# Performance work log

Hardware: AMD Instinct MI355X
Metric: run time of the kernel (lower is better)

Reference implementation:

```python
import jax, jax.numpy as jnp
import numpy as np

B, C, H, W = 8, 16, 64, 64
O = 32
K = 3
STRIDE = 1
HO = (H - K) // STRIDE + 1  # 62
WO = (W - K) // STRIDE + 1  # 62
BIAS_VAL = 0.1


def setup_inputs() -> dict:
    key = jax.random.key(0)
    k1, k2 = jax.random.split(key)
    x = jax.random.normal(k1, (B, C, H, W), dtype=jnp.float32)
    # per-location weights: (1, O, C, Ho, Wo, K*K) in torch; drop leading 1
    weight = jax.random.normal(k2, (O, C, HO, WO, K * K), dtype=jnp.float32)
    bias = jnp.full((1, O, HO, WO), BIAS_VAL, dtype=jnp.float32)
    return {"x": x, "weight": weight, "bias": bias}


def _extract_patches(x):
    # emulate x.unfold(2,K,S).unfold(3,K,S).reshape(..., K*K)
    # patch index k = ki*K + kj
    patches = [
        x[:, :, ki:ki + (HO - 1) * STRIDE + 1:STRIDE, kj:kj + (WO - 1) * STRIDE + 1:STRIDE]
        for ki in range(K) for kj in range(K)
    ]
    return jnp.stack(patches, axis=-1)  # [B, C, Ho, Wo, K*K]


def reference(x, weight, bias):
    patches = _extract_patches(x)  # [B, C, Ho, Wo, K2]
    # (x.unsqueeze(1) * weight).sum([2, -1]) == contraction over C and K2 per location
    out = jnp.einsum('bchwk,ochwk->bohw', patches, weight)
    return out + bias
```

## Files before the change

### kernel.cpp

```cpp
#include <hip/hip_runtime.h>


#define BB 8
#define CC 16
#define HH 64
#define WW 64
#define OO 32
#define HO 62
#define WO 62
#define NLOC (HO * WO)
#define TOTAL (OO * NLOC)

typedef float f4 __attribute__((ext_vector_type(4)));
typedef float f2 __attribute__((ext_vector_type(2)));

__device__ __forceinline__ void async_f32_to_lds(const float* g, float* l) {
  __builtin_amdgcn_global_load_lds((const __attribute__((address_space(1))) void*)g,
                                   (__attribute__((address_space(3))) void*)l,
                                   4, 0, 0);
}

__global__ __launch_bounds__(256) void lc2d_kernel(
    const float* __restrict__ x, const float* __restrict__ weight,
    const float* __restrict__ bias, float* __restrict__ out) {
  __shared__ float smem[4 * 2 * 576];

  const int tid  = threadIdx.x;
  const int lane = tid & 63;
  const int wave = tid >> 6;
  const int l = lane & 15;
  const int q = lane >> 4;
  const int ho = blockIdx.x % HO;
  const int o  = blockIdx.x / HO;

  float* buf0 = smem + wave * 1152;
  float* buf1 = buf0 + 576;

  const int colbase = 4 * l;
  const int f2off = (l < 15) ? 4 : -4;

  const float* wbase = weight + (size_t)(o * CC + wave * 4) * (NLOC * 9)
                              + (size_t)ho * (WO * 9);

#pragma unroll
  for (int j = 0; j < 9; ++j)
    if (j * 64 + lane < WO * 9)
      async_f32_to_lds(wbase + j * 64 + lane, buf0 + j * 64);

  f4 acc[2];
  acc[0] = (f4)0.f;
  acc[1] = (f4)0.f;

  __syncthreads();

  float* cur = buf0;
  float* nxt = buf1;

  for (int cc = 0; cc < 4; ++cc) {
    if (cc < 3) {
      const float* wg = wbase + (size_t)(cc + 1) * (NLOC * 9);
#pragma unroll
      for (int j = 0; j < 9; ++j)
        if (j * 64 + lane < WO * 9)
          async_f32_to_lds(wg + j * 64 + lane, nxt + j * 64);
    }

    f4 wq[9];
#pragma unroll
    for (int k = 0; k < 9; ++k)
      wq[k] = *(const f4*)(cur + 36 * l + 4 * k);

    const int c = wave * 4 + cc;

#pragma unroll
    for (int bo = 0; bo < 2; ++bo) {
      const int b = 2 * q + bo;
      const float* xb = x + ((size_t)b * CC + c) * (HH * WW)
                          + (size_t)ho * WW + colbase;
      f4 v4[3];
      f2 v2[3];
#pragma unroll
      for (int r = 0; r < 3; ++r) {
        v4[r] = *(const f4*)(xb + r * WW);
        v2[r] = *(const f2*)(xb + r * WW + f2off);
      }
#pragma unroll
      for (int w4 = 0; w4 < 4; ++w4) {
        float s = 0.f;
#pragma unroll
        for (int r = 0; r < 3; ++r) {
#pragma unroll
          for (int j = 0; j < 3; ++j) {
            const int e = w4 + j;
            const int wi = w4 * 9 + r * 3 + j;
            const float xv = (e < 4) ? v4[r][e] : v2[r][e - 4];
            s += xv * wq[wi >> 2][wi & 3];
          }
        }
        acc[bo][w4] += s;
      }
    }

    __syncthreads();
    float* t = cur; cur = nxt; nxt = t;
  }

#pragma unroll
  for (int bo = 0; bo < 2; ++bo)
    *(f4*)(buf0 + (2 * q + bo) * 64 + colbase) = acc[bo];
  __syncthreads();

  for (int p = tid; p < 512; p += 256) {
    const int b  = p >> 6;
    const int wo = p & 63;
    if (wo < WO) {
      float s = smem[0 * 1152 + p] + smem[1 * 1152 + p]
              + smem[2 * 1152 + p] + smem[3 * 1152 + p];
      const int loc = o * NLOC + ho * WO + wo;
      out[(size_t)b * TOTAL + loc] = s + bias[loc];
    }
  }
}

extern "C" void kernel_launch(void* const* d_in, const int* in_sizes, int n_in,
                              void* d_out, int out_size, void* d_ws, size_t ws_size,
                              hipStream_t stream) {
  const float* x = (const float*)d_in[0];
  const float* w = (const float*)d_in[1];
  const float* bias = (const float*)d_in[2];
  float* out = (float*)d_out;

  hipLaunchKernelGGL(lc2d_kernel, dim3(OO * HO), dim3(256), 0, stream,
                     x, w, bias, out);
}
```

Before: 26.61 us.

## Prefetch all four channel weight slices into LDS and drop per-iteration barriers

Result: slower. 49.14 us (+84.7%).

```diff
diff --git a/kernel.cpp b/kernel.cpp
--- a/kernel.cpp
+++ b/kernel.cpp
@@ -20,10 +20,10 @@
                                    4, 0, 0);
 }
 
-__global__ __launch_bounds__(256) void lc2d_kernel(
+__global__ __launch_bounds__(256, 4) void lc2d_kernel(
     const float* __restrict__ x, const float* __restrict__ weight,
     const float* __restrict__ bias, float* __restrict__ out) {
-  __shared__ float smem[4 * 2 * 576];
+  __shared__ __align__(16) float smem[4 * 4 * 576];
 
   const int tid  = threadIdx.x;
   const int lane = tid & 63;
@@ -33,9 +33,7 @@
   const int ho = blockIdx.x % HO;
   const int o  = blockIdx.x / HO;
 
-  float* buf0 = smem + wave * 1152;
-  float* buf1 = buf0 + 576;
-
+  float* bufs = smem + wave * 2304;
   const int colbase = 4 * l;
   const int f2off = (l < 15) ? 4 : -4;
 
@@ -43,79 +41,72 @@
                               + (size_t)ho * (WO * 9);
 
 #pragma unroll
-  for (int j = 0; j < 9; ++j)
-    if (j * 64 + lane < WO * 9)
-      async_f32_to_lds(wbase + j * 64 + lane, buf0 + j * 64);
+  for (int cc = 0; cc < 4; ++cc) {
+    const float* wg = wbase + (size_t)cc * (NLOC * 9);
+    float* dst = bufs + cc * 576;
+#pragma unroll
+    for (int j = 0; j < 9; ++j)
+      if (j * 64 + lane < WO * 9)
+        async_f32_to_lds(wg + j * 64 + lane, dst + j * 64);
+  }
 
   f4 acc[2];
   acc[0] = (f4)0.f;
   acc[1] = (f4)0.f;
 
-  __syncthreads();
+#define BODY(cc, WAITSTR)                                                     \
+  {                                                                           \
+    asm volatile("s_waitcnt " WAITSTR ::: "memory");                          \
+    const float* cur = bufs + (cc) * 576;                                     \
+    f4 wq[9];                                                                 \
+    _Pragma("unroll")                                                         \
+    for (int k = 0; k < 9; ++k) wq[k] = *(const f4*)(cur + 36 * l + 4 * k);   \
+    const float* xc = x + (size_t)(wave * 4 + (cc)) * (HH * WW)               \
+                        + (size_t)ho * WW + colbase;                          \
+    _Pragma("unroll")                                                         \
+    for (int bo = 0; bo < 2; ++bo) {                                          \
+      const float* xb = xc + (size_t)(2 * q + bo) * (CC * HH * WW);           \
+      f4 v4[3]; f2 v2[3];                                                     \
+      _Pragma("unroll")                                                       \
+      for (int r = 0; r < 3; ++r) {                                           \
+        v4[r] = *(const f4*)(xb + r * WW);                                    \
+        v2[r] = *(const f2*)(xb + r * WW + f2off);                            \
+      }                                                                       \
+      _Pragma("unroll")                                                       \
+      for (int w4 = 0; w4 < 4; ++w4) {                                        \
+        float s = 0.f;                                                        \
+        _Pragma("unroll")                                                     \
+        for (int r = 0; r < 3; ++r) {                                         \
+          _Pragma("unroll")                                                   \
+          for (int j = 0; j < 3; ++j) {                                       \
+            const int e = w4 + j;                     \
+            const int wi = w4 * 9 + r * 3 + j;       \
+            const float xv = (e < 4) ? v4[r][e] : v2[r][e - 4];               \
+            s += xv * wq[wi >> 2][wi & 3];                                    \
+          }                                                                   \
+        }                                                                     \
+        acc[bo][w4] += s;                                                     \
+      }                                                                       \
+    }                                                                         \
+  }
 
-  float* cur = buf0;
-  float* nxt = buf1;
-
-  for (int cc = 0; cc < 4; ++cc) {
-    if (cc < 3) {
-      const float* wg = wbase + (size_t)(cc + 1) * (NLOC * 9);
-#pragma unroll
-      for (int j = 0; j < 9; ++j)
-        if (j * 64 + lane < WO * 9)
-          async_f32_to_lds(wg + j * 64 + lane, nxt + j * 64);
-    }
-
-    f4 wq[9];
-#pragma unroll
-    for (int k = 0; k < 9; ++k)
-      wq[k] = *(const f4*)(cur + 36 * l + 4 * k);
-
-    const int c = wave * 4 + cc;
-
-#pragma unroll
-    for (int bo = 0; bo < 2; ++bo) {
-      const int b = 2 * q + bo;
-      const float* xb = x + ((size_t)b * CC + c) * (HH * WW)
-                          + (size_t)ho * WW + colbase;
-      f4 v4[3];
-      f2 v2[3];
-#pragma unroll
-      for (int r = 0; r < 3; ++r) {
-        v4[r] = *(const f4*)(xb + r * WW);
-        v2[r] = *(const f2*)(xb + r * WW + f2off);
-      }
-#pragma unroll
-      for (int w4 = 0; w4 < 4; ++w4) {
-        float s = 0.f;
-#pragma unroll
-        for (int r = 0; r < 3; ++r) {
-#pragma unroll
-          for (int j = 0; j < 3; ++j) {
-            const int e = w4 + j;
-            const int wi = w4 * 9 + r * 3 + j;
-            const float xv = (e < 4) ? v4[r][e] : v2[r][e - 4];
-            s += xv * wq[wi >> 2][wi & 3];
-          }
-        }
-        acc[bo][w4] += s;
-      }
-    }
-
-    __syncthreads();
-    float* t = cur; cur = nxt; nxt = t;
-  }
+  BODY(0, "vmcnt(27)")
+  BODY(1, "vmcnt(18)")
+  BODY(2, "vmcnt(9)")
+  BODY(3, "vmcnt(0)")
+#undef BODY
 
 #pragma unroll
   for (int bo = 0; bo < 2; ++bo)
-    *(f4*)(buf0 + (2 * q + bo) * 64 + colbase) = acc[bo];
+    *(f4*)(bufs + (2 * q + bo) * 64 + colbase) = acc[bo];
   __syncthreads();
 
   for (int p = tid; p < 512; p += 256) {
     const int b  = p >> 6;
     const int wo = p & 63;
     if (wo < WO) {
-      float s = smem[0 * 1152 + p] + smem[1 * 1152 + p]
-              + smem[2 * 1152 + p] + smem[3 * 1152 + p];
+      float s = smem[0 * 2304 + p] + smem[1 * 2304 + p]
+              + smem[2 * 2304 + p] + smem[3 * 2304 + p];
       const int loc = o * NLOC + ho * WO + wo;
       out[(size_t)b * TOTAL + loc] = s + bias[loc];
     }
```
